# Kernel tuning notes

Measured on AMD Instinct MI355X. Metric: run time of the kernel, lower is better.

Reference implementation:

```python
import jax, jax.numpy as jnp
import numpy as np

N, E, F, H, C, G = 100000, 1600000, 128, 4, 32, 64
D = H * C  # 128, per-layer node dim
NEG_SLOPE = 0.2
BN_EPS = 1e-5


def setup_inputs() -> dict:
    key = jax.random.key(0)
    ks = jax.random.split(key, 24)
    inp = {
        "x": jax.random.normal(ks[0], (N, F), jnp.float32),
        "edge_index": jax.random.randint(ks[1], (2, E), 0, N, jnp.int64),
        "batch": jnp.sort(jax.random.randint(ks[2], (N,), 0, G, jnp.int64)),
        # GATConv layer 0: in=F, out=C per head
        "w0": jax.random.normal(ks[3], (F, H * C), jnp.float32) * 0.1,
        "att_src0": jax.random.normal(ks[4], (H, C), jnp.float32) * 0.1,
        "att_dst0": jax.random.normal(ks[5], (H, C), jnp.float32) * 0.1,
        "bias0": jax.random.normal(ks[6], (H * C,), jnp.float32) * 0.1,
        # GATConv layer 1: in=D, out=C per head
        "w1": jax.random.normal(ks[7], (D, H * C), jnp.float32) * 0.1,
        "att_src1": jax.random.normal(ks[8], (H, C), jnp.float32) * 0.1,
        "att_dst1": jax.random.normal(ks[9], (H, C), jnp.float32) * 0.1,
        "bias1": jax.random.normal(ks[10], (H * C,), jnp.float32) * 0.1,
        # BatchNorm (eval mode: running stats)
        "bn_g0": jax.random.normal(ks[11], (D,), jnp.float32) * 0.1 + 1.0,
        "bn_b0": jax.random.normal(ks[12], (D,), jnp.float32) * 0.1,
        "bn_m0": jax.random.normal(ks[13], (D,), jnp.float32) * 0.1,
        "bn_v0": jax.random.uniform(ks[14], (D,), jnp.float32) + 0.5,
        "bn_g1": jax.random.normal(ks[15], (D,), jnp.float32) * 0.1 + 1.0,
        "bn_b1": jax.random.normal(ks[16], (D,), jnp.float32) * 0.1,
        "bn_m1": jax.random.normal(ks[17], (D,), jnp.float32) * 0.1,
        "bn_v1": jax.random.uniform(ks[18], (D,), jnp.float32) + 0.5,
        # head MLP
        "lin1_w": jax.random.normal(ks[19], (D, D // 2), jnp.float32) * 0.1,
        "lin1_b": jax.random.normal(ks[20], (D // 2,), jnp.float32) * 0.1,
        "lin2_w": jax.random.normal(ks[21], (D // 2, 1), jnp.float32) * 0.1,
        "lin2_b": jax.random.normal(ks[22], (1,), jnp.float32) * 0.1,
    }
    return inp


def gat_conv(x, src, dst, w, att_s, att_d, bias):
    """PyG GATConv (concat=True, add_self_loops already in src/dst), eval mode."""
    n = x.shape[0]
    h = (x @ w).reshape(n, H, C)                       # [N,H,C]
    a_s = jnp.sum(h * att_s, axis=-1)                   # [N,H]
    a_d = jnp.sum(h * att_d, axis=-1)                   # [N,H]
    e = jax.nn.leaky_relu(a_s[src] + a_d[dst], NEG_SLOPE)  # [Etot,H]
    m = jax.ops.segment_max(e, dst, num_segments=n)
    m = jax.lax.stop_gradient(jnp.where(jnp.isfinite(m), m, 0.0))
    ex = jnp.exp(e - m[dst])
    denom = jax.ops.segment_sum(ex, dst, num_segments=n)
    alpha = ex / (denom[dst] + 1e-16)                    # segment softmax over dst
    out = jax.ops.segment_sum(h[src] * alpha[:, :, None], dst, num_segments=n)
    return out.reshape(n, H * C) + bias


def bn_eval(x, g, b, m, v):
    return (x - m) * jax.lax.rsqrt(v + BN_EPS) * g + b


def reference(x, edge_index, batch,
              w0, att_src0, att_dst0, bias0,
              w1, att_src1, att_dst1, bias1,
              bn_g0, bn_b0, bn_m0, bn_v0,
              bn_g1, bn_b1, bn_m1, bn_v1,
              lin1_w, lin1_b, lin2_w, lin2_b):
    n = x.shape[0]
    loops = jnp.arange(n, dtype=edge_index.dtype)
    src = jnp.concatenate([edge_index[0], loops])
    dst = jnp.concatenate([edge_index[1], loops])

    h = gat_conv(x, src, dst, w0, att_src0, att_dst0, bias0)
    h = jax.nn.relu(bn_eval(h, bn_g0, bn_b0, bn_m0, bn_v0))
    h = gat_conv(h, src, dst, w1, att_src1, att_dst1, bias1)
    h = jax.nn.relu(bn_eval(h, bn_g1, bn_b1, bn_m1, bn_v1))

    # global mean pool over graphs
    summed = jax.ops.segment_sum(h, batch, num_segments=G)           # [G,D]
    counts = jax.ops.segment_sum(jnp.ones((n,), h.dtype), batch, num_segments=G)
    pooled = summed / jnp.maximum(counts, 1.0)[:, None]

    z = jax.nn.relu(pooled @ lin1_w + lin1_b)
    return z @ lin2_w + lin2_b                                        # [G,1]
```

## Files before the change

### kernel.cpp

```cpp
#include <hip/hip_runtime.h>

#define GG 64
#define STRIDE 10240
#define NBINMAX 256

typedef __attribute__((ext_vector_type(8))) short short8;
typedef __attribute__((ext_vector_type(4))) float f32x4;


__device__ inline unsigned short bf16rne(float f) {
  unsigned int x = __float_as_uint(f);
  unsigned int r = (x + 0x7FFFu + ((x >> 16) & 1u)) >> 16;
  return (unsigned short)r;
}
__device__ inline unsigned int pack2(float a, float b) {
  return (unsigned int)bf16rne(a) | ((unsigned int)bf16rne(b) << 16);
}
__device__ inline float blo(unsigned int v) { return __uint_as_float(v << 16); }
__device__ inline float bhi(unsigned int v) { return __uint_as_float(v & 0xFFFF0000u); }


__global__ __launch_bounds__(256) void init_gcur(int* __restrict__ gcur) {
  gcur[threadIdx.x] = threadIdx.x * STRIDE;
}

__global__ __launch_bounds__(256) void part_p1(const int* __restrict__ ei,
                                               int* __restrict__ gcur,
                                               unsigned int* __restrict__ pairs,
                                               int E, int N) {
  __shared__ int hist[NBINMAX];
  __shared__ int gbase[NBINMAX];
  __shared__ int lcur[NBINMAX];
  int t = threadIdx.x;
  int tot = E + N;
  int base = blockIdx.x * 4096;
  hist[t] = 0;
  __syncthreads();
  int sarr[16], darr[16];
  #pragma unroll
  for (int k = 0; k < 16; ++k) {
    int i = base + k * 256 + t;
    if (i < tot) {
      int s, d;
      if (i < E) { s = ei[i]; d = ei[E + i]; } else { s = i - E; d = s; }
      sarr[k] = s; darr[k] = d;
      atomicAdd(&hist[d >> 9], 1);
    } else darr[k] = -1;
  }
  __syncthreads();
  int c = hist[t];
  gbase[t] = (c > 0) ? atomicAdd(&gcur[t], c) : 0;
  lcur[t] = 0;
  __syncthreads();
  #pragma unroll
  for (int k = 0; k < 16; ++k) {
    int d = darr[k];
    if (d >= 0) {
      int b = d >> 9;
      int p = gbase[b] + atomicAdd(&lcur[b], 1);
      pairs[p] = ((unsigned int)(d & 511) << 17) | (unsigned int)sarr[k];
    }
  }
}


__global__ __launch_bounds__(256) void part_p2(const unsigned int* __restrict__ pairs,
                                               const int* __restrict__ gcur,
                                               int* __restrict__ ssrc,
                                               int* __restrict__ offsets,
                                               int* __restrict__ counts, int N) {
  __shared__ int ncnt[512], ncur[512], excl_s[512];
  __shared__ int wsum[4];
  int b = blockIdx.x;
  int t = threadIdx.x;
  int pb = b * STRIDE;
  int cnt = gcur[b] - pb;
  ncnt[t] = 0; ncnt[t + 256] = 0;
  __syncthreads();
  for (int e = t; e < cnt; e += 256) {
    unsigned int v = pairs[pb + e];
    atomicAdd(&ncnt[v >> 17], 1);
  }
  __syncthreads();
  int c0 = ncnt[2 * t], c1 = ncnt[2 * t + 1];
  int ps = c0 + c1;
  int lane = t & 63, w = t >> 6;
  int x = ps;
  #pragma unroll
  for (int s = 1; s < 64; s <<= 1) { int y = __shfl_up(x, s); if (lane >= s) x += y; }
  if (lane == 63) wsum[w] = x;
  __syncthreads();
  int woff = 0;
  for (int i = 0; i < w; ++i) woff += wsum[i];
  int ep = woff + x - ps;
  excl_s[2 * t]     = ep;
  excl_s[2 * t + 1] = ep + c0;
  __syncthreads();
  int binstart = b << 9;
  for (int i = t; i < 512; i += 256) {
    ncur[i] = excl_s[i];
    int node = binstart + i;
    if (node < N) { offsets[node] = pb + excl_s[i]; counts[node] = ncnt[i]; }
  }
  __syncthreads();
  for (int e = t; e < cnt; e += 256) {
    unsigned int v = pairs[pb + e];
    int dl = v >> 17;
    int p = atomicAdd(&ncur[dl], 1);
    ssrc[pb + p] = (int)(v & 0x1FFFF);
  }
}


__global__ __launch_bounds__(256) void gbounds(const int* __restrict__ batch,
                                               int* __restrict__ gstart, int N) {
  int i = blockIdx.x * 256 + threadIdx.x;
  if (i >= N) return;
  int g = batch[i];
  if (i == 0 || batch[i - 1] != g) gstart[g] = i;
}

__global__ void gfix(const int* __restrict__ gstart, int* __restrict__ go,
                     int* __restrict__ ge, int N) {
  if (threadIdx.x == 0 && blockIdx.x == 0) {
    int nxt = N;
    for (int g = GG - 1; g >= 0; --g) {
      int s = gstart[g];
      if (s < 0) { go[g] = nxt; ge[g] = nxt; }
      else       { go[g] = s;   ge[g] = nxt; nxt = s; }
    }
  }
}


__global__ __launch_bounds__(256) void wprep(const float* __restrict__ w0,
                                             const float* __restrict__ w1,
                                             unsigned short* __restrict__ wt) {
  int idx = blockIdx.x * 256 + threadIdx.x;
  int layer = idx >> 14;
  int e = idx & 16383;
  int k = e >> 7, n = e & 127;
  float v = (layer ? w1 : w0)[e];
  unsigned short hi = bf16rne(v);
  float hif = __uint_as_float((unsigned int)hi << 16);
  unsigned short lo = bf16rne(v - hif);
  unsigned short* basep = wt + layer * 32768;
  basep[n * 128 + k] = hi;
  basep[16384 + n * 128 + k] = lo;
}


__global__ __launch_bounds__(256) void gemm_mfma(
    const float* __restrict__ in, const unsigned short* __restrict__ wtL,
    const float* __restrict__ att_s, const float* __restrict__ att_d,
    unsigned int* __restrict__ h16, float* __restrict__ a_s,
    float* __restrict__ a_d, int N) {
  __shared__ unsigned short xh[128][40], xl[128][40];
  __shared__ unsigned short bh[128][40], bl[128][40];
  int t = threadIdx.x;
  int base = blockIdx.x * 128;
  int lane = t & 63, wv = t >> 6;
  int l15 = lane & 15, lg = lane >> 4;
  int n0 = wv * 32;

  f32x4 zero4 = {0.f, 0.f, 0.f, 0.f};
  f32x4 acc[8][2];
  #pragma unroll
  for (int rt = 0; rt < 8; ++rt) { acc[rt][0] = zero4; acc[rt][1] = zero4; }

  int sr = t >> 1;
  int sc = (t & 1) * 16;
  int gr = base + sr;
  int rc = gr < N ? gr : (N - 1);
  const float* xp = &in[(size_t)rc * 128 + sc];
  const unsigned short* whp = &wtL[(size_t)sr * 128 + sc];
  const unsigned short* wlp = whp + 16384;

  for (int kt = 0; kt < 4; ++kt) {
    int k0 = kt * 32;
    __syncthreads();
    #pragma unroll
    for (int q = 0; q < 4; ++q) {
      float4 u = *(const float4*)(xp + k0 + q * 4);
      unsigned short h0 = bf16rne(u.x), h1 = bf16rne(u.y);
      unsigned short h2 = bf16rne(u.z), h3 = bf16rne(u.w);
      float f0 = __uint_as_float((unsigned)h0 << 16);
      float f1 = __uint_as_float((unsigned)h1 << 16);
      float f2 = __uint_as_float((unsigned)h2 << 16);
      float f3 = __uint_as_float((unsigned)h3 << 16);
      *(unsigned int*)&xh[sr][sc + q * 4]     = (unsigned)h0 | ((unsigned)h1 << 16);
      *(unsigned int*)&xh[sr][sc + q * 4 + 2] = (unsigned)h2 | ((unsigned)h3 << 16);
      *(unsigned int*)&xl[sr][sc + q * 4]     =
          (unsigned)bf16rne(u.x - f0) | ((unsigned)bf16rne(u.y - f1) << 16);
      *(unsigned int*)&xl[sr][sc + q * 4 + 2] =
          (unsigned)bf16rne(u.z - f2) | ((unsigned)bf16rne(u.w - f3) << 16);
    }
    {
      uint4 a0 = *(const uint4*)(whp + k0);
      uint4 a1 = *(const uint4*)(whp + k0 + 8);
      *(uint4*)&bh[sr][sc]     = a0;
      *(uint4*)&bh[sr][sc + 8] = a1;
      uint4 b0 = *(const uint4*)(wlp + k0);
      uint4 b1 = *(const uint4*)(wlp + k0 + 8);
      *(uint4*)&bl[sr][sc]     = b0;
      *(uint4*)&bl[sr][sc + 8] = b1;
    }
    __syncthreads();
    short8 fbh0 = *(const short8*)&bh[n0 + l15][lg * 8];
    short8 fbh1 = *(const short8*)&bh[n0 + 16 + l15][lg * 8];
    short8 fbl0 = *(const short8*)&bl[n0 + l15][lg * 8];
    short8 fbl1 = *(const short8*)&bl[n0 + 16 + l15][lg * 8];
    #pragma unroll
    for (int rt = 0; rt < 8; ++rt) {
      short8 fah = *(const short8*)&xh[rt * 16 + l15][lg * 8];
      short8 fal = *(const short8*)&xl[rt * 16 + l15][lg * 8];
      acc[rt][0] = __builtin_amdgcn_mfma_f32_16x16x32_bf16(fah, fbh0, acc[rt][0], 0, 0, 0);
      acc[rt][1] = __builtin_amdgcn_mfma_f32_16x16x32_bf16(fah, fbh1, acc[rt][1], 0, 0, 0);
      acc[rt][0] = __builtin_amdgcn_mfma_f32_16x16x32_bf16(fal, fbh0, acc[rt][0], 0, 0, 0);
      acc[rt][1] = __builtin_amdgcn_mfma_f32_16x16x32_bf16(fal, fbh1, acc[rt][1], 0, 0, 0);
      acc[rt][0] = __builtin_amdgcn_mfma_f32_16x16x32_bf16(fah, fbl0, acc[rt][0], 0, 0, 0);
      acc[rt][1] = __builtin_amdgcn_mfma_f32_16x16x32_bf16(fah, fbl1, acc[rt][1], 0, 0, 0);
    }
  }

  float as0 = att_s[n0 + l15], as1 = att_s[n0 + 16 + l15];
  float ad0 = att_d[n0 + l15], ad1 = att_d[n0 + 16 + l15];
  #pragma unroll
  for (int rt = 0; rt < 8; ++rt) {
    float ps[4], pd[4];
    #pragma unroll
    for (int q = 0; q < 4; ++q) {
      float c0v = acc[rt][0][q], c1v = acc[rt][1][q];
      float p0 = __shfl_xor(c0v, 1), p1 = __shfl_xor(c1v, 1);
      int row = base + rt * 16 + lg * 4 + q;
      if (!(l15 & 1) && row < N) {
        h16[(size_t)row * 64 + (n0 + l15) / 2]      = pack2(c0v, p0);
        h16[(size_t)row * 64 + (n0 + 16 + l15) / 2] = pack2(c1v, p1);
      }
      ps[q] = c0v * as0 + c1v * as1;
      pd[q] = c0v * ad0 + c1v * ad1;
    }
    #pragma unroll
    for (int m = 1; m <= 8; m <<= 1) {
      #pragma unroll
      for (int q = 0; q < 4; ++q) { ps[q] += __shfl_xor(ps[q], m); pd[q] += __shfl_xor(pd[q], m); }
    }
    if (l15 == 0) {
      #pragma unroll
      for (int q = 0; q < 4; ++q) {
        int row = base + rt * 16 + lg * 4 + q;
        if (row < N) { a_s[row * 4 + wv] = ps[q]; a_d[row * 4 + wv] = pd[q]; }
      }
    }
  }
}


#define ACCP(EX, V0, V1)                                                       \
  { float2 ex2 = make_float2(EX, EX);                                          \
    acc2[0] += ex2 * make_float2(blo(V0.x), bhi(V0.x));                        \
    acc2[1] += ex2 * make_float2(blo(V0.y), bhi(V0.y));                        \
    acc2[2] += ex2 * make_float2(blo(V0.z), bhi(V0.z));                        \
    acc2[3] += ex2 * make_float2(blo(V0.w), bhi(V0.w));                        \
    acc2[4] += ex2 * make_float2(blo(V1.x), bhi(V1.x));                        \
    acc2[5] += ex2 * make_float2(blo(V1.y), bhi(V1.y));                        \
    acc2[6] += ex2 * make_float2(blo(V1.z), bhi(V1.z));                        \
    acc2[7] += ex2 * make_float2(blo(V1.w), bhi(V1.w)); }

__global__ __launch_bounds__(256) void gat_aggregate(
    const unsigned int* __restrict__ h16, const float* __restrict__ a_s, const float* __restrict__ a_d,
    const int* __restrict__ offsets, const int* __restrict__ counts, const int* __restrict__ ssrc,
    const float* __restrict__ bias,
    const float* __restrict__ bn_g, const float* __restrict__ bn_b,
    const float* __restrict__ bn_m, const float* __restrict__ bn_v,
    float* __restrict__ out, int N) {
  __shared__ float part[4][8][132];
  int wv = threadIdx.x >> 6;
  int lane = threadIdx.x & 63;
  int wid = blockIdx.x * 4 + wv;
  if (wid >= N) return;
  int off = offsets[wid], cnt = counts[wid];
  int eg = lane >> 3;
  int j  = lane & 7;
  int hh = j >> 1;
  float ad = a_d[wid * 4 + hh];

  float2 acc2[8] = {};
  float den = 0.f;

  int sA = ssrc[off + (eg < cnt ? eg : 0)];
  int iB0 = eg + 8;
  int sB = ssrc[off + (iB0 < cnt ? iB0 : 0)];
  float asA = a_s[sA * 4 + hh];
  float asB = a_s[sB * 4 + hh];

  for (int i = eg; i < cnt; i += 16) {
    const uint4* hpA = (const uint4*)(h16 + (size_t)sA * 64 + j * 8);
    uint4 va0 = hpA[0], va1 = hpA[1];
    const uint4* hpB = (const uint4*)(h16 + (size_t)sB * 64 + j * 8);
    uint4 vb0 = hpB[0], vb1 = hpB[1];
    int in0 = i + 16, in1 = i + 24;
    int snA = ssrc[off + (in0 < cnt ? in0 : 0)];
    int snB = ssrc[off + (in1 < cnt ? in1 : 0)];
    float anA = a_s[snA * 4 + hh];
    float anB = a_s[snB * 4 + hh];
    float eA = asA + ad; eA = eA > 0.f ? eA : 0.2f * eA;
    float exA = __expf(eA);
    float eB = asB + ad; eB = eB > 0.f ? eB : 0.2f * eB;
    float exB = ((i + 8) < cnt) ? __expf(eB) : 0.f;
    den += exA + exB;
    ACCP(exA, va0, va1)
    ACCP(exB, vb0, vb1)
    sA = snA; sB = snB; asA = anA; asB = anB;
  }

  den += __shfl_xor(den, 8);
  den += __shfl_xor(den, 16);
  den += __shfl_xor(den, 32);
  den = __shfl(den, (lane >> 4) * 2);

  float* pw = &part[wv][eg][j * 16];
  *(float4*)(pw + 0)  = make_float4(acc2[0].x, acc2[0].y, acc2[1].x, acc2[1].y);
  *(float4*)(pw + 4)  = make_float4(acc2[2].x, acc2[2].y, acc2[3].x, acc2[3].y);
  *(float4*)(pw + 8)  = make_float4(acc2[4].x, acc2[4].y, acc2[5].x, acc2[5].y);
  *(float4*)(pw + 12) = make_float4(acc2[6].x, acc2[6].y, acc2[7].x, acc2[7].y);
  asm volatile("s_waitcnt lgkmcnt(0)" ::: "memory");

  int d = lane * 2;
  float r0 = 0.f, r1 = 0.f;
  #pragma unroll
  for (int g = 0; g < 8; ++g) {
    float2 v = *(const float2*)(&part[wv][g][d]);
    r0 += v.x; r1 += v.y;
  }

  float inv = 1.f / (den + 1e-16f);
  float2 bi = *(const float2*)(&bias[d]);
  float2 g2 = *(const float2*)(&bn_g[d]);
  float2 b2 = *(const float2*)(&bn_b[d]);
  float2 m2 = *(const float2*)(&bn_m[d]);
  float2 v2 = *(const float2*)(&bn_v[d]);
  float o0 = r0 * inv + bi.x;
  float o1 = r1 * inv + bi.y;
  o0 = fmaxf((o0 - m2.x) * (g2.x * rsqrtf(v2.x + 1e-5f)) + b2.x, 0.f);
  o1 = fmaxf((o1 - m2.y) * (g2.y * rsqrtf(v2.y + 1e-5f)) + b2.y, 0.f);
  *(float2*)(&out[(size_t)wid * 128 + d]) = make_float2(o0, o1);
}


#define POOLP 8

__global__ __launch_bounds__(256) void pool_kernel(const float* __restrict__ y,
                                                   const int* __restrict__ go,
                                                   const int* __restrict__ ge,
                                                   float* __restrict__ pooled) {
  int g = blockIdx.x / POOLP, p = blockIdx.x % POOLP;
  int s = go[g], e = ge[g];
  int len = e - s;
  int q0 = s + (len * p) / POOLP, q1 = s + (len * (p + 1)) / POOLP;
  int t = threadIdx.x;
  int d = t & 127, half = t >> 7;
  float acc = 0.f;
  for (int i = q0 + half; i < q1; i += 2) acc += y[(size_t)i * 128 + d];
  __shared__ float red[256];
  red[t] = acc;
  __syncthreads();
  if (half == 0) atomicAdd(&pooled[g * 128 + d], red[d] + red[d + 128]);
}

__global__ __launch_bounds__(64) void mlp_kernel(const float* __restrict__ pooled,
                                                 const int* __restrict__ go,
                                                 const int* __restrict__ ge,
                                                 const float* __restrict__ w1,
                                                 const float* __restrict__ b1,
                                                 const float* __restrict__ w2,
                                                 const float* __restrict__ b2,
                                                 float* __restrict__ out) {
  int g = blockIdx.x, j = threadIdx.x;
  int cnt = ge[g] - go[g];
  float inv = 1.f / (float)(cnt > 1 ? cnt : 1);
  float z = b1[j];
  for (int k = 0; k < 128; ++k) z += pooled[g * 128 + k] * inv * w1[k * 64 + j];
  z = fmaxf(z, 0.f);
  float v = z * w2[j];
  #pragma unroll
  for (int m = 1; m < 64; m <<= 1) v += __shfl_xor(v, m);
  if (j == 0) out[g] = v + b2[0];
}


extern "C" void kernel_launch(void* const* d_in, const int* in_sizes, int n_in,
                              void* d_out, int out_size, void* d_ws, size_t ws_size,
                              hipStream_t stream) {
  const float* x     = (const float*)d_in[0];
  const int*   ei    = (const int*)d_in[1];
  const int*   batch = (const int*)d_in[2];
  const float* w0    = (const float*)d_in[3];
  const float* atts0 = (const float*)d_in[4];
  const float* attd0 = (const float*)d_in[5];
  const float* bias0 = (const float*)d_in[6];
  const float* w1    = (const float*)d_in[7];
  const float* atts1 = (const float*)d_in[8];
  const float* attd1 = (const float*)d_in[9];
  const float* bias1 = (const float*)d_in[10];
  const float* bng0  = (const float*)d_in[11];
  const float* bnb0  = (const float*)d_in[12];
  const float* bnm0  = (const float*)d_in[13];
  const float* bnv0  = (const float*)d_in[14];
  const float* bng1  = (const float*)d_in[15];
  const float* bnb1  = (const float*)d_in[16];
  const float* bnm1  = (const float*)d_in[17];
  const float* bnv1  = (const float*)d_in[18];
  const float* l1w   = (const float*)d_in[19];
  const float* l1b   = (const float*)d_in[20];
  const float* l2w   = (const float*)d_in[21];
  const float* l2b   = (const float*)d_in[22];

  int N = in_sizes[2];
  int E = in_sizes[1] / 2;
  int tot = E + N;
  int NBIN = (N + 511) / 512;

  char* p = (char*)d_ws;
  unsigned int* h16 = (unsigned int*)p; p += (size_t)N * 128 * 2;
  float* y_buf  = (float*)p; p += (size_t)N * 128 * 4;
  float* a_s    = (float*)p; p += (size_t)N * 4 * 4;
  float* a_d    = (float*)p; p += (size_t)N * 4 * 4;
  int* counts   = (int*)p;   p += (size_t)N * 4;
  int* offsets  = (int*)p;   p += (size_t)N * 4;
  int* ssrc     = (int*)p;   p += (size_t)NBINMAX * STRIDE * 4;
  int* gcur     = (int*)p;   p += NBINMAX * 4;
  int* gstart   = (int*)p;   p += 64 * 4;
  int* go       = (int*)p;   p += 64 * 4;
  int* ge       = (int*)p;   p += 64 * 4;
  float* pooled = (float*)p; p += 64 * 128 * 4;
  unsigned short* wt = (unsigned short*)p; p += 2 * 32768 * 2;
  unsigned int* pairs = (unsigned int*)y_buf;

  hipMemsetAsync(gstart, 0xFF, 64 * 4, stream);
  hipMemsetAsync(pooled, 0, 64 * 128 * 4, stream);

  int bN = (N + 255) / 256;
  int bW = (N + 3) / 4;
  int bG = (N + 127) / 128;

  init_gcur<<<1, 256, 0, stream>>>(gcur);
  part_p1<<<(tot + 4095) / 4096, 256, 0, stream>>>(ei, gcur, pairs, E, N);
  part_p2<<<NBIN, 256, 0, stream>>>(pairs, gcur, ssrc, offsets, counts, N);
  gbounds<<<bN, 256, 0, stream>>>(batch, gstart, N);
  gfix<<<1, 64, 0, stream>>>(gstart, go, ge, N);
  wprep<<<128, 256, 0, stream>>>(w0, w1, wt);

  gemm_mfma<<<bG, 256, 0, stream>>>(x, wt, atts0, attd0, h16, a_s, a_d, N);
  gat_aggregate<<<bW, 256, 0, stream>>>(h16, a_s, a_d, offsets, counts, ssrc,
                                        bias0, bng0, bnb0, bnm0, bnv0, y_buf, N);
  gemm_mfma<<<bG, 256, 0, stream>>>(y_buf, wt + 32768, atts1, attd1, h16, a_s, a_d, N);
  gat_aggregate<<<bW, 256, 0, stream>>>(h16, a_s, a_d, offsets, counts, ssrc,
                                        bias1, bng1, bnb1, bnm1, bnv1, y_buf, N);
  pool_kernel<<<GG * POOLP, 256, 0, stream>>>(y_buf, go, ge, pooled);
  mlp_kernel<<<GG, 64, 0, stream>>>(pooled, go, ge, l1w, l1b, l2w, l2b, (float*)d_out);
}
```

Before: 334.3 us.

## Split GEMM output columns across blocks and prefetch next K-tile into registers

The node-feature GEMM now launches two blocks per 128-row tile, each computing half of the output columns, so each wave handles 64 rows by 32 columns. Weight fragments are read straight from global memory into registers, which removes the shared-memory weight tiles. The next K-slice of activations and weights is loaded during the current MFMA work, overlapping global-load latency with compute. In exchange, every input row is read and split into bf16 hi/lo halves twice, once per column half.

```diff
diff --git a/kernel.cpp b/kernel.cpp
--- a/kernel.cpp
+++ b/kernel.cpp
@@ -156,83 +156,102 @@
     unsigned int* __restrict__ h16, float* __restrict__ a_s,
     float* __restrict__ a_d, int N) {
   __shared__ unsigned short xh[128][40], xl[128][40];
-  __shared__ unsigned short bh[128][40], bl[128][40];
   int t = threadIdx.x;
-  int base = blockIdx.x * 128;
-  int lane = t & 63, wv = t >> 6;
+  int bid = blockIdx.x;
+  int ch = bid & 1;
+  int base = (bid >> 1) * 128;
+  int lane = t & 63, w = t >> 6;
   int l15 = lane & 15, lg = lane >> 4;
-  int n0 = wv * 32;
+  int hd = w & 1;
+  int n0 = ch * 64 + hd * 32;
+  int rh = w >> 1;
 
   f32x4 zero4 = {0.f, 0.f, 0.f, 0.f};
-  f32x4 acc[8][2];
-  #pragma unroll
-  for (int rt = 0; rt < 8; ++rt) { acc[rt][0] = zero4; acc[rt][1] = zero4; }
+  f32x4 acc[4][2];
+  #pragma unroll
+  for (int rt = 0; rt < 4; ++rt) { acc[rt][0] = zero4; acc[rt][1] = zero4; }
 
   int sr = t >> 1;
   int sc = (t & 1) * 16;
   int gr = base + sr;
   int rc = gr < N ? gr : (N - 1);
   const float* xp = &in[(size_t)rc * 128 + sc];
-  const unsigned short* whp = &wtL[(size_t)sr * 128 + sc];
-  const unsigned short* wlp = whp + 16384;
-
+
+  const unsigned short* wh0 = &wtL[(size_t)(n0 + l15) * 128];
+  const unsigned short* wh1 = &wtL[(size_t)(n0 + 16 + l15) * 128];
+
+  float4 u0 = *(const float4*)(xp + 0);
+  float4 u1 = *(const float4*)(xp + 4);
+  float4 u2 = *(const float4*)(xp + 8);
+  float4 u3 = *(const float4*)(xp + 12);
+  short8 cbh0 = *(const short8*)(wh0 + lg * 8);
+  short8 cbh1 = *(const short8*)(wh1 + lg * 8);
+  short8 cbl0 = *(const short8*)(wh0 + 16384 + lg * 8);
+  short8 cbl1 = *(const short8*)(wh1 + 16384 + lg * 8);
+
+  #pragma unroll
   for (int kt = 0; kt < 4; ++kt) {
-    int k0 = kt * 32;
+    if (kt) __syncthreads();
+    {
+      float4 uu[4] = {u0, u1, u2, u3};
+      #pragma unroll
+      for (int q = 0; q < 4; ++q) {
+        float4 u = uu[q];
+        unsigned short h0 = bf16rne(u.x), h1 = bf16rne(u.y);
+        unsigned short h2 = bf16rne(u.z), h3 = bf16rne(u.w);
+        float f0 = __uint_as_float((unsigned)h0 << 16);
+        float f1 = __uint_as_float((unsigned)h1 << 16);
+        float f2 = __uint_as_float((unsigned)h2 << 16);
+        float f3 = __uint_as_float((unsigned)h3 << 16);
+        *(unsigned int*)&xh[sr][sc + q * 4]     = (unsigned)h0 | ((unsigned)h1 << 16);
+        *(unsigned int*)&xh[sr][sc + q * 4 + 2] = (unsigned)h2 | ((unsigned)h3 << 16);
+        *(unsigned int*)&xl[sr][sc + q * 4]     =
+            (unsigned)bf16rne(u.x - f0) | ((unsigned)bf16rne(u.y - f1) << 16);
+        *(unsigned int*)&xl[sr][sc + q * 4 + 2] =
+            (unsigned)bf16rne(u.z - f2) | ((unsigned)bf16rne(u.w - f3) << 16);
+      }
+    }
     __syncthreads();
+    float4 v0 = u0, v1 = u1, v2 = u2, v3 = u3;
+    short8 nbh0 = cbh0, nbh1 = cbh1, nbl0 = cbl0, nbl1 = cbl1;
+    if (kt < 3) {
+      int k1 = (kt + 1) * 32;
+      v0 = *(const float4*)(xp + k1);
+      v1 = *(const float4*)(xp + k1 + 4);
+      v2 = *(const float4*)(xp + k1 + 8);
+      v3 = *(const float4*)(xp + k1 + 12);
+      nbh0 = *(const short8*)(wh0 + k1 + lg * 8);
+      nbh1 = *(const short8*)(wh1 + k1 + lg * 8);
+      nbl0 = *(const short8*)(wh0 + 16384 + k1 + lg * 8);
+      nbl1 = *(const short8*)(wh1 + 16384 + k1 + lg * 8);
+    }
     #pragma unroll
-    for (int q = 0; q < 4; ++q) {
-      float4 u = *(const float4*)(xp + k0 + q * 4);
-      unsigned short h0 = bf16rne(u.x), h1 = bf16rne(u.y);
-      unsigned short h2 = bf16rne(u.z), h3 = bf16rne(u.w);
-      float f0 = __uint_as_float((unsigned)h0 << 16);
-      float f1 = __uint_as_float((unsigned)h1 << 16);
-      float f2 = __uint_as_float((unsigned)h2 << 16);
-      float f3 = __uint_as_float((unsigned)h3 << 16);
-      *(unsigned int*)&xh[sr][sc + q * 4]     = (unsigned)h0 | ((unsigned)h1 << 16);
-      *(unsigned int*)&xh[sr][sc + q * 4 + 2] = (unsigned)h2 | ((unsigned)h3 << 16);
-      *(unsigned int*)&xl[sr][sc + q * 4]     =
-          (unsigned)bf16rne(u.x - f0) | ((unsigned)bf16rne(u.y - f1) << 16);
-      *(unsigned int*)&xl[sr][sc + q * 4 + 2] =
-          (unsigned)bf16rne(u.z - f2) | ((unsigned)bf16rne(u.w - f3) << 16);
-    }
-    {
-      uint4 a0 = *(const uint4*)(whp + k0);
-      uint4 a1 = *(const uint4*)(whp + k0 + 8);
-      *(uint4*)&bh[sr][sc]     = a0;
-      *(uint4*)&bh[sr][sc + 8] = a1;
-      uint4 b0 = *(const uint4*)(wlp + k0);
-      uint4 b1 = *(const uint4*)(wlp + k0 + 8);
-      *(uint4*)&bl[sr][sc]     = b0;
-      *(uint4*)&bl[sr][sc + 8] = b1;
-    }
-    __syncthreads();
-    short8 fbh0 = *(const short8*)&bh[n0 + l15][lg * 8];
-    short8 fbh1 = *(const short8*)&bh[n0 + 16 + l15][lg * 8];
-    short8 fbl0 = *(const short8*)&bl[n0 + l15][lg * 8];
-    short8 fbl1 = *(const short8*)&bl[n0 + 16 + l15][lg * 8];
-    #pragma unroll
-    for (int rt = 0; rt < 8; ++rt) {
-      short8 fah = *(const short8*)&xh[rt * 16 + l15][lg * 8];
-      short8 fal = *(const short8*)&xl[rt * 16 + l15][lg * 8];
-      acc[rt][0] = __builtin_amdgcn_mfma_f32_16x16x32_bf16(fah, fbh0, acc[rt][0], 0, 0, 0);
-      acc[rt][1] = __builtin_amdgcn_mfma_f32_16x16x32_bf16(fah, fbh1, acc[rt][1], 0, 0, 0);
-      acc[rt][0] = __builtin_amdgcn_mfma_f32_16x16x32_bf16(fal, fbh0, acc[rt][0], 0, 0, 0);
-      acc[rt][1] = __builtin_amdgcn_mfma_f32_16x16x32_bf16(fal, fbh1, acc[rt][1], 0, 0, 0);
-      acc[rt][0] = __builtin_amdgcn_mfma_f32_16x16x32_bf16(fah, fbl0, acc[rt][0], 0, 0, 0);
-      acc[rt][1] = __builtin_amdgcn_mfma_f32_16x16x32_bf16(fah, fbl1, acc[rt][1], 0, 0, 0);
-    }
-  }
-
+    for (int rt = 0; rt < 4; ++rt) {
+      int row = rh * 64 + rt * 16 + l15;
+      short8 fah = *(const short8*)&xh[row][lg * 8];
+      short8 fal = *(const short8*)&xl[row][lg * 8];
+      acc[rt][0] = __builtin_amdgcn_mfma_f32_16x16x32_bf16(fah, cbh0, acc[rt][0], 0, 0, 0);
+      acc[rt][1] = __builtin_amdgcn_mfma_f32_16x16x32_bf16(fah, cbh1, acc[rt][1], 0, 0, 0);
+      acc[rt][0] = __builtin_amdgcn_mfma_f32_16x16x32_bf16(fal, cbh0, acc[rt][0], 0, 0, 0);
+      acc[rt][1] = __builtin_amdgcn_mfma_f32_16x16x32_bf16(fal, cbh1, acc[rt][1], 0, 0, 0);
+      acc[rt][0] = __builtin_amdgcn_mfma_f32_16x16x32_bf16(fah, cbl0, acc[rt][0], 0, 0, 0);
+      acc[rt][1] = __builtin_amdgcn_mfma_f32_16x16x32_bf16(fah, cbl1, acc[rt][1], 0, 0, 0);
+    }
+    u0 = v0; u1 = v1; u2 = v2; u3 = v3;
+    cbh0 = nbh0; cbh1 = nbh1; cbl0 = nbl0; cbl1 = nbl1;
+  }
+
+  int headg = ch * 2 + hd;
   float as0 = att_s[n0 + l15], as1 = att_s[n0 + 16 + l15];
   float ad0 = att_d[n0 + l15], ad1 = att_d[n0 + 16 + l15];
   #pragma unroll
-  for (int rt = 0; rt < 8; ++rt) {
+  for (int rt = 0; rt < 4; ++rt) {
     float ps[4], pd[4];
     #pragma unroll
     for (int q = 0; q < 4; ++q) {
       float c0v = acc[rt][0][q], c1v = acc[rt][1][q];
       float p0 = __shfl_xor(c0v, 1), p1 = __shfl_xor(c1v, 1);
-      int row = base + rt * 16 + lg * 4 + q;
+      int row = base + rh * 64 + rt * 16 + lg * 4 + q;
       if (!(l15 & 1) && row < N) {
         h16[(size_t)row * 64 + (n0 + l15) / 2]      = pack2(c0v, p0);
         h16[(size_t)row * 64 + (n0 + 16 + l15) / 2] = pack2(c1v, p1);
@@ -248,8 +267,8 @@
     if (l15 == 0) {
       #pragma unroll
       for (int q = 0; q < 4; ++q) {
-        int row = base + rt * 16 + lg * 4 + q;
-        if (row < N) { a_s[row * 4 + wv] = ps[q]; a_d[row * 4 + wv] = pd[q]; }
+        int row = base + rh * 64 + rt * 16 + lg * 4 + q;
+        if (row < N) { a_s[row * 4 + headg] = ps[q]; a_d[row * 4 + headg] = pd[q]; }
       }
     }
   }
@@ -442,7 +461,7 @@
 
   int bN = (N + 255) / 256;
   int bW = (N + 3) / 4;
-  int bG = (N + 127) / 128;
+  int bG2 = 2 * ((N + 127) / 128);
 
   init_gcur<<<1, 256, 0, stream>>>(gcur);
   part_p1<<<(tot + 4095) / 4096, 256, 0, stream>>>(ei, gcur, pairs, E, N);
@@ -451,10 +470,10 @@
   gfix<<<1, 64, 0, stream>>>(gstart, go, ge, N);
   wprep<<<128, 256, 0, stream>>>(w0, w1, wt);
 
-  gemm_mfma<<<bG, 256, 0, stream>>>(x, wt, atts0, attd0, h16, a_s, a_d, N);
+  gemm_mfma<<<bG2, 256, 0, stream>>>(x, wt, atts0, attd0, h16, a_s, a_d, N);
   gat_aggregate<<<bW, 256, 0, stream>>>(h16, a_s, a_d, offsets, counts, ssrc,
                                         bias0, bng0, bnb0, bnm0, bnv0, y_buf, N);
-  gemm_mfma<<<bG, 256, 0, stream>>>(y_buf, wt + 32768, atts1, attd1, h16, a_s, a_d, N);
+  gemm_mfma<<<bG2, 256, 0, stream>>>(y_buf, wt + 32768, atts1, attd1, h16, a_s, a_d, N);
   gat_aggregate<<<bW, 256, 0, stream>>>(h16, a_s, a_d, offsets, counts, ssrc,
                                         bias1, bng1, bnb1, bnm1, bnv1, y_buf, N);
   pool_kernel<<<GG * POOLP, 256, 0, stream>>>(y_buf, go, ge, pooled);
```

Measured after the change: 328.2 us. Within noise of the previous version (-1.8%).
